# Kernel tuning notes

Hardware: AMD Instinct MI355X
Metric: run time of the kernel (lower is better)

The kernel has to match this reference:

```python
import math
import jax, jax.numpy as jnp
import numpy as np

B, L, H = 8, 2048, 256


def setup_inputs() -> dict:
    key = jax.random.key(0)
    k1, k2, k3, k4, k5 = jax.random.split(key, 5)
    inputs = jax.random.normal(k1, (B, L, H), dtype=jnp.float32)
    scale = 1.0 / math.sqrt(H)
    Wq = jax.random.normal(k2, (H, H), dtype=jnp.float32) * scale
    Wk = jax.random.normal(k3, (H, H), dtype=jnp.float32) * scale
    Wv = jax.random.normal(k4, (H, H), dtype=jnp.float32) * scale
    lens = jax.random.randint(k5, (B,), L // 2, L + 1)
    lens = lens.at[0].set(L)  # original assumes max(lens) == L
    return {"inputs": inputs, "Wq": Wq, "Wk": Wk, "Wv": Wv, "lens": lens}


def reference(inputs, Wq, Wk, Wv, lens):
    # nn.Linear(bias=False): y = x @ W.T
    Q = jnp.einsum('blh,oh->blo', inputs, Wq)
    K = jnp.einsum('blh,oh->blo', inputs, Wk)
    V = jnp.einsum('blh,oh->blo', inputs, Wv)
    d = Q.shape[-1]
    alpha = jnp.einsum('bqd,bkd->bqk', Q, K) / math.sqrt(d)  # [B, L, L]
    # key-padding mask: [B, 1, L] broadcast over query dim (matches expand)
    mask = (jnp.arange(L)[None, :] < lens[:, None])[:, None, :]
    NEG = jnp.float32(-2.0 ** 31)
    alpha = jnp.where(mask, alpha, NEG)
    alpha = jax.nn.softmax(alpha, axis=2)
    out = jnp.einsum('bqk,bkd->bqd', alpha, V)
    return out
```

## Files before the change

kernel.cpp:

```cpp
#include <hip/hip_runtime.h>

#define BB 8
#define LL 2048
#define DD 256

typedef _Float16 half8 __attribute__((ext_vector_type(8)));
typedef float floatx4 __attribute__((ext_vector_type(4)));
typedef unsigned short ushort8 __attribute__((ext_vector_type(8)));

__device__ inline unsigned short f2h(float f) {
  _Float16 h = (_Float16)f;
  return __builtin_bit_cast(unsigned short, h);
}

__global__ __launch_bounds__(256) void wcvt(
    const float* __restrict__ Wq, const float* __restrict__ Wk,
    const float* __restrict__ Wv, unsigned short* __restrict__ Wh) {
  const int bm = blockIdx.x >> 5;
  const float* src = (bm == 0) ? Wq : (bm == 1) ? Wk : Wv;
  const int off = (blockIdx.x & 31) * 2048 + threadIdx.x * 8;
  float4 a = *(const float4*)(src + off);
  float4 b = *(const float4*)(src + off + 4);
  ushort8 u = {f2h(a.x), f2h(a.y), f2h(a.z), f2h(a.w),
               f2h(b.x), f2h(b.y), f2h(b.z), f2h(b.w)};
  *(ushort8*)(Wh + bm * 65536 + off) = u;
}

__global__ __launch_bounds__(256) void proj(
    const float* __restrict__ x, const unsigned short* __restrict__ Wh,
    unsigned short* __restrict__ Qb, unsigned short* __restrict__ Kb,
    unsigned short* __restrict__ VT) {
  const int t = threadIdx.x;
  const int wave = t >> 6, lane = t & 63, quad = lane >> 4, m16 = lane & 15;
  const int l0g = blockIdx.x * 32;
  const int b = l0g >> 11, lb = l0g & 2047;

  half8 xf[2][8];
  for (int mt = 0; mt < 2; ++mt) {
    const float* xp = x + (size_t)(l0g + mt * 16 + m16) * DD + quad * 8;
    for (int kb = 0; kb < 8; ++kb) {
      float4 a = *(const float4*)(xp + kb * 32);
      float4 c = *(const float4*)(xp + kb * 32 + 4);
      ushort8 u = {f2h(a.x), f2h(a.y), f2h(a.z), f2h(a.w),
                   f2h(c.x), f2h(c.y), f2h(c.z), f2h(c.w)};
      xf[mt][kb] = __builtin_bit_cast(half8, u);
    }
  }

  for (int j = 0; j < 12; ++j) {
    const int nt = wave * 12 + j;
    const int mat = nt >> 4, ot = nt & 15;
    const unsigned short* wp =
        Wh + mat * 65536 + (ot * 16 + m16) * DD + quad * 8;
    floatx4 acc[2] = {{0, 0, 0, 0}, {0, 0, 0, 0}};
    if (mat < 2) {
      for (int kb = 0; kb < 8; ++kb) {
        half8 wf = __builtin_bit_cast(half8, *(const ushort8*)(wp + kb * 32));
        acc[0] = __builtin_amdgcn_mfma_f32_16x16x32_f16(xf[0][kb], wf, acc[0], 0, 0, 0);
        acc[1] = __builtin_amdgcn_mfma_f32_16x16x32_f16(xf[1][kb], wf, acc[1], 0, 0, 0);
      }
      unsigned short* Out = mat ? Kb : Qb;
      for (int mt = 0; mt < 2; ++mt)
        for (int r = 0; r < 4; ++r)
          Out[(size_t)(l0g + mt * 16 + quad * 4 + r) * DD + ot * 16 + m16] =
              f2h(acc[mt][r]);
    } else {
      for (int kb = 0; kb < 8; ++kb) {
        half8 wf = __builtin_bit_cast(half8, *(const ushort8*)(wp + kb * 32));
        acc[0] = __builtin_amdgcn_mfma_f32_16x16x32_f16(wf, xf[0][kb], acc[0], 0, 0, 0);
        acc[1] = __builtin_amdgcn_mfma_f32_16x16x32_f16(wf, xf[1][kb], acc[1], 0, 0, 0);
      }
      for (int mt = 0; mt < 2; ++mt)
        for (int r = 0; r < 4; ++r)
          VT[((size_t)(b * DD + ot * 16 + quad * 4 + r)) * LL + lb + mt * 16 +
             m16] = f2h(acc[mt][r]);
    }
  }
}

__global__ __launch_bounds__(512, 2) void attn(
    const unsigned short* __restrict__ Qb, const unsigned short* __restrict__ Kb,
    const unsigned short* __restrict__ VT, const int* __restrict__ lens,
    float* __restrict__ out) {
  __shared__ __attribute__((aligned(16))) unsigned char smem[149504];
  const int t = threadIdx.x;
  const int wave = t >> 6, lane = t & 63, quad = lane >> 4, m16 = lane & 15;
  const int grp = wave >> 2, qw = wave & 3, tgl = t & 255;
  unsigned short* Ks = (unsigned short*)(smem + grp * 32768);
  unsigned short* Vs = (unsigned short*)(smem + 65536 + grp * 32768);
  unsigned short* Pw = (unsigned short*)(smem + 131072 + wave * 2304);

  const int b = blockIdx.y;
  const int q0 = blockIdx.x * 64;
  const int len = lens[b];
  const size_t baseQK = (size_t)b * LL * DD;
  const size_t baseVT = (size_t)b * DD * LL;

  half8 qf[8];
  {
    const unsigned short* qrow =
        Qb + baseQK + (size_t)(q0 + qw * 16 + m16) * DD + quad * 8;
    for (int kb = 0; kb < 8; ++kb)
      qf[kb] = __builtin_bit_cast(half8, *(const ushort8*)(qrow + kb * 32));
  }

  floatx4 O[16];
  for (int i = 0; i < 16; ++i) O[i] = (floatx4){0, 0, 0, 0};
  float mrow[4] = {-1e30f, -1e30f, -1e30f, -1e30f};
  float lrow[4] = {0.f, 0.f, 0.f, 0.f};

  ushort8 kreg[8], vreg[8];
  const unsigned short* kbase = Kb + baseQK;
  const unsigned short* vbase = VT + baseVT;

#define LOAD_TILES(KV0)                                                      \
  {                                                                          \
    const unsigned short* kp = kbase + (size_t)(KV0)*DD;                     \
    for (int c = 0; c < 8; ++c)                                              \
      kreg[c] = *(const ushort8*)(kp + (tgl + c * 256) * 8);                 \
    for (int c = 0; c < 8; ++c) {                                            \
      int ch = tgl + c * 256;                                                \
      vreg[c] = *(const ushort8*)(vbase + (size_t)(ch >> 3) * LL + (KV0) +   \
                                  (ch & 7) * 8);                             \
    }                                                                        \
  }

  const int T = (len + 127) >> 7;
  LOAD_TILES(grp * 64);

  for (int it = 0; it < T; ++it) {
    const int kv0 = it * 128 + grp * 64;
    __syncthreads();
    for (int c = 0; c < 8; ++c) {
      int ch = tgl + c * 256, row = ch >> 5, cc = ch & 31;
      *(ushort8*)&Ks[row * 256 + (cc ^ (row & 7)) * 8] = kreg[c];
    }
    for (int c = 0; c < 8; ++c) {
      int ch = tgl + c * 256, d = ch >> 3, cc = ch & 7;
      *(ushort8*)&Vs[d * 64 + (cc ^ (d & 7)) * 8] = vreg[c];
    }
    __syncthreads();
    if (it + 1 < T) LOAD_TILES(kv0 + 128);

    if (kv0 < len) {
      floatx4 s[4];
      for (int n = 0; n < 4; ++n) s[n] = (floatx4){0, 0, 0, 0};
      for (int kb = 0; kb < 8; ++kb)
        for (int n = 0; n < 4; ++n) {
          half8 kf = __builtin_bit_cast(
              half8, *(const ushort8*)&Ks[(n * 16 + m16) * 256 +
                                          (((kb * 4 + quad) ^ (m16 & 7)) * 8)]);
          s[n] = __builtin_amdgcn_mfma_f32_16x16x32_f16(qf[kb], kf, s[n], 0, 0, 0);
        }
      float sv[4][4];
      for (int n = 0; n < 4; ++n) {
        bool valid = (kv0 + n * 16 + m16) < len;
        for (int r = 0; r < 4; ++r)
          sv[n][r] = valid ? s[n][r] * 0.0625f : -1e30f;
      }
      float al[4];
      for (int r = 0; r < 4; ++r) {
        float v = fmaxf(fmaxf(sv[0][r], sv[1][r]), fmaxf(sv[2][r], sv[3][r]));
        v = fmaxf(v, __shfl_xor(v, 1));
        v = fmaxf(v, __shfl_xor(v, 2));
        v = fmaxf(v, __shfl_xor(v, 4));
        v = fmaxf(v, __shfl_xor(v, 8));
        float mn = fmaxf(mrow[r], v);
        al[r] = __expf(mrow[r] - mn);
        mrow[r] = mn;
        float sum = 0.f;
        for (int n = 0; n < 4; ++n) {
          float p = __expf(sv[n][r] - mn);
          Pw[(quad * 4 + r) * 72 + n * 16 + m16] = f2h(p);
          sum += p;
        }
        sum += __shfl_xor(sum, 1);
        sum += __shfl_xor(sum, 2);
        sum += __shfl_xor(sum, 4);
        sum += __shfl_xor(sum, 8);
        lrow[r] = lrow[r] * al[r] + sum;
      }
      for (int i = 0; i < 16; ++i)
        for (int r = 0; r < 4; ++r) O[i][r] *= al[r];
      half8 pf0 = __builtin_bit_cast(half8,
                                     *(const ushort8*)&Pw[m16 * 72 + quad * 8]);
      half8 pf1 = __builtin_bit_cast(
          half8, *(const ushort8*)&Pw[m16 * 72 + 32 + quad * 8]);
      for (int nb = 0; nb < 16; ++nb) {
        half8 vf0 = __builtin_bit_cast(
            half8, *(const ushort8*)&Vs[(nb * 16 + m16) * 64 +
                                        ((quad ^ (m16 & 7)) * 8)]);
        O[nb] = __builtin_amdgcn_mfma_f32_16x16x32_f16(pf0, vf0, O[nb], 0, 0, 0);
        half8 vf1 = __builtin_bit_cast(
            half8, *(const ushort8*)&Vs[(nb * 16 + m16) * 64 +
                                        (((4 + quad) ^ (m16 & 7)) * 8)]);
        O[nb] = __builtin_amdgcn_mfma_f32_16x16x32_f16(pf1, vf1, O[nb], 0, 0, 0);
      }
    }
  }
#undef LOAD_TILES

  __syncthreads();
  float* Om = (float*)(smem) + qw * 4112;
  float* ml = (float*)(smem + 65792) + qw * 32;
  if (grp == 1) {
    for (int nb = 0; nb < 16; ++nb)
      for (int r = 0; r < 4; ++r)
        Om[(quad * 4 + r) * 257 + nb * 16 + m16] = O[nb][r];
    if (m16 == 0)
      for (int r = 0; r < 4; ++r) {
        ml[(quad * 4 + r) * 2] = mrow[r];
        ml[(quad * 4 + r) * 2 + 1] = lrow[r];
      }
  }
  __syncthreads();
  if (grp == 0) {
    float a[4], bf[4], inv[4];
    for (int r = 0; r < 4; ++r) {
      float mB = ml[(quad * 4 + r) * 2];
      float lB = ml[(quad * 4 + r) * 2 + 1];
      float m = fmaxf(mrow[r], mB);
      a[r] = __expf(mrow[r] - m);
      bf[r] = __expf(mB - m);
      inv[r] = 1.f / (lrow[r] * a[r] + lB * bf[r]);
    }
    for (int nb = 0; nb < 16; ++nb)
      for (int r = 0; r < 4; ++r) {
        float ob = Om[(quad * 4 + r) * 257 + nb * 16 + m16];
        out[baseQK + (size_t)(q0 + qw * 16 + quad * 4 + r) * DD + nb * 16 +
            m16] = (O[nb][r] * a[r] + ob * bf[r]) * inv[r];
      }
  }
}

extern "C" void kernel_launch(void* const* d_in, const int* in_sizes, int n_in,
                              void* d_out, int out_size, void* d_ws, size_t ws_size,
                              hipStream_t stream) {
  const float* x = (const float*)d_in[0];
  const float* Wq = (const float*)d_in[1];
  const float* Wk = (const float*)d_in[2];
  const float* Wv = (const float*)d_in[3];
  const int* lens = (const int*)d_in[4];
  unsigned short* Qb = (unsigned short*)d_ws;
  unsigned short* Kb = Qb + (size_t)BB * LL * DD;
  unsigned short* VT = Kb + (size_t)BB * LL * DD;
  unsigned short* Wh = VT + (size_t)BB * LL * DD;
  float* out = (float*)d_out;

  wcvt<<<96, 256, 0, stream>>>(Wq, Wk, Wv, Wh);
  proj<<<512, 256, 0, stream>>>(x, Wh, Qb, Kb, VT);
  attn<<<dim3(32, 8), 512, 0, stream>>>(Qb, Kb, VT, lens, out);
}
```

Baseline: 194.2 us.

## Shrink attention blocks to 32 queries and 32-key tiles, skip no-op rescale

The attention kernel now uses 256-thread blocks, each handling 32 queries with two KV groups of 32 keys per iteration, which doubles the grid to 512 blocks and roughly halves shared memory per block. The intent is better CU coverage and occupancy on a 256-CU part, since the previous 256-block grid left the device underfilled. The O rescale is skipped when all alpha factors are exactly one, tested with a wave ballot. In exchange, K/V are reloaded from global memory twice as often across blocks, the V tile swizzle is dropped (possible LDS bank conflicts), and there are more barriers per key.

```diff
diff --git a/kernel.cpp b/kernel.cpp
--- a/kernel.cpp
+++ b/kernel.cpp
@@ -78,20 +78,20 @@
   }
 }
 
-__global__ __launch_bounds__(512, 2) void attn(
+__global__ __launch_bounds__(256, 2) void attn(
     const unsigned short* __restrict__ Qb, const unsigned short* __restrict__ Kb,
     const unsigned short* __restrict__ VT, const int* __restrict__ lens,
     float* __restrict__ out) {
-  __shared__ __attribute__((aligned(16))) unsigned char smem[149504];
+  __shared__ __attribute__((aligned(16))) unsigned char smem[70656];
   const int t = threadIdx.x;
   const int wave = t >> 6, lane = t & 63, quad = lane >> 4, m16 = lane & 15;
-  const int grp = wave >> 2, qw = wave & 3, tgl = t & 255;
-  unsigned short* Ks = (unsigned short*)(smem + grp * 32768);
-  unsigned short* Vs = (unsigned short*)(smem + 65536 + grp * 32768);
-  unsigned short* Pw = (unsigned short*)(smem + 131072 + wave * 2304);
+  const int qw = wave & 1, grp = wave >> 1;
+  unsigned short* Ks = (unsigned short*)(smem + grp * 16384);
+  unsigned short* Vs = (unsigned short*)(smem + 32768 + grp * 16384);
+  unsigned short* Pw = (unsigned short*)(smem + 65536 + wave * 1280);
 
   const int b = blockIdx.y;
-  const int q0 = blockIdx.x * 64;
+  const int q0 = blockIdx.x * 32;
   const int len = lens[b];
   const size_t baseQK = (size_t)b * LL * DD;
   const size_t baseVT = (size_t)b * DD * LL;
@@ -113,54 +113,51 @@
   const unsigned short* kbase = Kb + baseQK;
   const unsigned short* vbase = VT + baseVT;
 
-#define LOAD_TILES(KV0)                                                      \
-  {                                                                          \
-    const unsigned short* kp = kbase + (size_t)(KV0)*DD;                     \
-    for (int c = 0; c < 8; ++c)                                              \
-      kreg[c] = *(const ushort8*)(kp + (tgl + c * 256) * 8);                 \
-    for (int c = 0; c < 8; ++c) {                                            \
-      int ch = tgl + c * 256;                                                \
-      vreg[c] = *(const ushort8*)(vbase + (size_t)(ch >> 3) * LL + (KV0) +   \
-                                  (ch & 7) * 8);                             \
-    }                                                                        \
-  }
-
-  const int T = (len + 127) >> 7;
-  LOAD_TILES(grp * 64);
+#define LOAD_TILES(KV0)                                                       \
+  {                                                                           \
+    for (int c = 0; c < 8; ++c) {                                             \
+      int ch = qw * 512 + c * 64 + lane;                                      \
+      kreg[c] = *(const ushort8*)(kbase + (size_t)((KV0) + (ch >> 5)) * DD +  \
+                                  (ch & 31) * 8);                             \
+      vreg[c] = *(const ushort8*)(vbase + (size_t)(ch >> 2) * LL + (KV0) +    \
+                                  (ch & 3) * 8);                              \
+    }                                                                         \
+  }
+
+  const int T = (len + 63) >> 6;
+  LOAD_TILES(grp * 32);
 
   for (int it = 0; it < T; ++it) {
-    const int kv0 = it * 128 + grp * 64;
+    const int kv0 = it * 64 + grp * 32;
     __syncthreads();
     for (int c = 0; c < 8; ++c) {
-      int ch = tgl + c * 256, row = ch >> 5, cc = ch & 31;
-      *(ushort8*)&Ks[row * 256 + (cc ^ (row & 7)) * 8] = kreg[c];
-    }
-    for (int c = 0; c < 8; ++c) {
-      int ch = tgl + c * 256, d = ch >> 3, cc = ch & 7;
-      *(ushort8*)&Vs[d * 64 + (cc ^ (d & 7)) * 8] = vreg[c];
+      int ch = qw * 512 + c * 64 + lane;
+      int row = ch >> 5, cc = ch & 31;
+      *(ushort8*)&Ks[row * 256 + ((cc ^ (row & 7)) * 8)] = kreg[c];
+      int d = ch >> 2, c2 = ch & 3;
+      *(ushort8*)&Vs[d * 32 + c2 * 8] = vreg[c];
     }
     __syncthreads();
-    if (it + 1 < T) LOAD_TILES(kv0 + 128);
+    if (it + 1 < T) LOAD_TILES(kv0 + 64);
 
     if (kv0 < len) {
-      floatx4 s[4];
-      for (int n = 0; n < 4; ++n) s[n] = (floatx4){0, 0, 0, 0};
+      floatx4 s[2] = {{0, 0, 0, 0}, {0, 0, 0, 0}};
       for (int kb = 0; kb < 8; ++kb)
-        for (int n = 0; n < 4; ++n) {
+        for (int n = 0; n < 2; ++n) {
           half8 kf = __builtin_bit_cast(
               half8, *(const ushort8*)&Ks[(n * 16 + m16) * 256 +
                                           (((kb * 4 + quad) ^ (m16 & 7)) * 8)]);
           s[n] = __builtin_amdgcn_mfma_f32_16x16x32_f16(qf[kb], kf, s[n], 0, 0, 0);
         }
-      float sv[4][4];
-      for (int n = 0; n < 4; ++n) {
+      float sv[2][4];
+      for (int n = 0; n < 2; ++n) {
         bool valid = (kv0 + n * 16 + m16) < len;
         for (int r = 0; r < 4; ++r)
           sv[n][r] = valid ? s[n][r] * 0.0625f : -1e30f;
       }
       float al[4];
       for (int r = 0; r < 4; ++r) {
-        float v = fmaxf(fmaxf(sv[0][r], sv[1][r]), fmaxf(sv[2][r], sv[3][r]));
+        float v = fmaxf(sv[0][r], sv[1][r]);
         v = fmaxf(v, __shfl_xor(v, 1));
         v = fmaxf(v, __shfl_xor(v, 2));
         v = fmaxf(v, __shfl_xor(v, 4));
@@ -169,9 +166,9 @@
         al[r] = __expf(mrow[r] - mn);
         mrow[r] = mn;
         float sum = 0.f;
-        for (int n = 0; n < 4; ++n) {
+        for (int n = 0; n < 2; ++n) {
           float p = __expf(sv[n][r] - mn);
-          Pw[(quad * 4 + r) * 72 + n * 16 + m16] = f2h(p);
+          Pw[(quad * 4 + r) * 40 + n * 16 + m16] = f2h(p);
           sum += p;
         }
         sum += __shfl_xor(sum, 1);
@@ -180,29 +177,25 @@
         sum += __shfl_xor(sum, 8);
         lrow[r] = lrow[r] * al[r] + sum;
       }
-      for (int i = 0; i < 16; ++i)
-        for (int r = 0; r < 4; ++r) O[i][r] *= al[r];
-      half8 pf0 = __builtin_bit_cast(half8,
-                                     *(const ushort8*)&Pw[m16 * 72 + quad * 8]);
-      half8 pf1 = __builtin_bit_cast(
-          half8, *(const ushort8*)&Pw[m16 * 72 + 32 + quad * 8]);
+      if (__ballot(al[0] != 1.f || al[1] != 1.f || al[2] != 1.f ||
+                   al[3] != 1.f)) {
+        for (int i = 0; i < 16; ++i)
+          for (int r = 0; r < 4; ++r) O[i][r] *= al[r];
+      }
+      half8 pf = __builtin_bit_cast(half8,
+                                    *(const ushort8*)&Pw[m16 * 40 + quad * 8]);
       for (int nb = 0; nb < 16; ++nb) {
-        half8 vf0 = __builtin_bit_cast(
-            half8, *(const ushort8*)&Vs[(nb * 16 + m16) * 64 +
-                                        ((quad ^ (m16 & 7)) * 8)]);
-        O[nb] = __builtin_amdgcn_mfma_f32_16x16x32_f16(pf0, vf0, O[nb], 0, 0, 0);
-        half8 vf1 = __builtin_bit_cast(
-            half8, *(const ushort8*)&Vs[(nb * 16 + m16) * 64 +
-                                        (((4 + quad) ^ (m16 & 7)) * 8)]);
-        O[nb] = __builtin_amdgcn_mfma_f32_16x16x32_f16(pf1, vf1, O[nb], 0, 0, 0);
+        half8 vf = __builtin_bit_cast(
+            half8, *(const ushort8*)&Vs[(nb * 16 + m16) * 32 + quad * 8]);
+        O[nb] = __builtin_amdgcn_mfma_f32_16x16x32_f16(pf, vf, O[nb], 0, 0, 0);
       }
     }
   }
 #undef LOAD_TILES
 
   __syncthreads();
-  float* Om = (float*)(smem) + qw * 4112;
-  float* ml = (float*)(smem + 65792) + qw * 32;
+  float* Om = (float*)smem + qw * 4112;
+  float* ml = (float*)(smem + 33024) + qw * 32;
   if (grp == 1) {
     for (int nb = 0; nb < 16; ++nb)
       for (int r = 0; r < 4; ++r)
@@ -249,5 +242,5 @@
 
   wcvt<<<96, 256, 0, stream>>>(Wq, Wk, Wv, Wh);
   proj<<<512, 256, 0, stream>>>(x, Wh, Qb, Kb, VT);
-  attn<<<dim3(32, 8), 512, 0, stream>>>(Qb, Kb, VT, lens, out);
-}
+  attn<<<dim3(64, 8), 256, 0, stream>>>(Qb, Kb, VT, lens, out);
+}
```

Result: slower. 217.6 us (+12.0%).
